# Kernel optimization log

Hardware: AMD Instinct MI355X
Metric: run time of the kernel (lower is better)

The kernel has to match this reference:

```python
import jax, jax.numpy as jnp
import numpy as np

N_NODES = 50000
N_EDGES = 800000
IN_CH = 128
HID = 32
HEADS = 4
OUT_CH = 16
NEG_SLOPE = 0.2  # PyG GATConv default LeakyReLU slope


def setup_inputs() -> dict:
    key = jax.random.key(0)
    ks = jax.random.split(key, 12)
    x = jax.random.normal(ks[0], (N_NODES, IN_CH), dtype=jnp.float32)
    edge_index = jax.random.randint(ks[1], (2, N_EDGES), 0, N_NODES, dtype=jnp.int32)
    edge_attr = jax.random.uniform(ks[2], (N_EDGES,), dtype=jnp.float32)
    s = 0.1
    W1 = jax.random.normal(ks[3], (IN_CH, HEADS * HID), dtype=jnp.float32) * s
    a_src1 = jax.random.normal(ks[4], (HEADS, HID), dtype=jnp.float32) * s
    a_dst1 = jax.random.normal(ks[5], (HEADS, HID), dtype=jnp.float32) * s
    b1 = jnp.zeros((HEADS * HID,), dtype=jnp.float32)
    W2 = jax.random.normal(ks[6], (HEADS * HID, OUT_CH), dtype=jnp.float32) * s
    a_src2 = jax.random.normal(ks[7], (1, OUT_CH), dtype=jnp.float32) * s
    a_dst2 = jax.random.normal(ks[8], (1, OUT_CH), dtype=jnp.float32) * s
    b2 = jnp.zeros((OUT_CH,), dtype=jnp.float32)
    return {"x": x, "edge_index": edge_index, "edge_attr": edge_attr,
            "W1": W1, "a_src1": a_src1, "a_dst1": a_dst1, "b1": b1,
            "W2": W2, "a_src2": a_src2, "a_dst2": a_dst2, "b2": b2}


def gat_conv(x, src, dst, num_nodes, W, a_src, a_dst, bias, concat):
    H, C = a_src.shape
    h = (x @ W).reshape(-1, H, C)              # [N,H,C]
    al_src = jnp.sum(h * a_src, axis=-1)       # [N,H]
    al_dst = jnp.sum(h * a_dst, axis=-1)       # [N,H]
    e = jax.nn.leaky_relu(al_src[src] + al_dst[dst], NEG_SLOPE)  # [E,H]
    # segment softmax over incoming edges of each destination node
    m = jax.ops.segment_max(e, dst, num_segments=num_nodes)
    ex = jnp.exp(e - m[dst])
    denom = jax.ops.segment_sum(ex, dst, num_segments=num_nodes)
    alpha = ex / (denom[dst] + 1e-16)          # [E,H]
    out = jax.ops.segment_sum(h[src] * alpha[..., None], dst, num_segments=num_nodes)  # [N,H,C]
    out = out.reshape(num_nodes, H * C) if concat else out.mean(axis=1)
    return out + bias


def reference(x, edge_index, edge_attr, W1, a_src1, a_dst1, b1, W2, a_src2, a_dst2, b2):
    # edge_attr is ignored by GATConv when edge_dim is None (PyG default)
    N = x.shape[0]
    loop = jnp.arange(N, dtype=edge_index.dtype)  # PyG add_self_loops=True
    src = jnp.concatenate([edge_index[0], loop])
    dst = jnp.concatenate([edge_index[1], loop])
    h = jax.nn.elu(gat_conv(x, src, dst, N, W1, a_src1, a_dst1, b1, True))
    out = gat_conv(h, src, dst, N, W2, a_src2, a_dst2, b2, False)
    return jax.nn.log_softmax(out, axis=1)
```

## Files before the change

kernel.cpp:

```cpp
#include <hip/hip_runtime.h>

#define N_NODESC 50000
#define E0C      800000
#define E_TOTC   850000
#define IN_CHC   128
#define HCC      128
#define HEADSC   4
#define OUT_CHC  16
#define NEG_SLOPE 0.2f
#define G1M      64
#define NG1      ((N_NODESC + G1M - 1)/G1M)
#define NBUCK    196
#define BNODES   256
#define SBLK     128
#define CHUNK    6656

typedef __attribute__((ext_vector_type(8))) short bf16x8;
typedef __attribute__((ext_vector_type(4))) float f32x4;

__device__ __forceinline__ float lrelu(float v){ return v > 0.f ? v : NEG_SLOPE * v; }

__device__ __forceinline__ unsigned int f2bf(float f){
  unsigned int b = __float_as_uint(f);
  return (b + 0x7fffu + ((b >> 16) & 1u)) >> 16;
}
__device__ __forceinline__ float bf2f(unsigned int lo16){
  return __uint_as_float(lo16 << 16);
}

__global__ void __launch_bounds__(256) k_gemm1A(const float* __restrict__ x, const float* __restrict__ W1,
        const float* __restrict__ a_s, const float* __restrict__ a_d,
        unsigned int* __restrict__ h1b, float* __restrict__ al_s, float* __restrict__ al_d,
        const int* __restrict__ ei, int* __restrict__ bh)
{
  __shared__ __align__(16) unsigned short Wt[IN_CHC*HCC];
  __shared__ __align__(16) unsigned short xt[G1M*IN_CHC];
  __shared__ int hh[NBUCK];
  int tid = threadIdx.x, lane = tid & 63, wave = tid >> 6;

  if (blockIdx.x >= NG1){
    int b = blockIdx.x - NG1;
    for (int i = tid; i < NBUCK; i += 256) hh[i] = 0;
    __syncthreads();
    int e0 = b*CHUNK, e1 = e0 + CHUNK; if (e1 > E_TOTC) e1 = E_TOTC;
    for (int e = e0 + tid; e < e1; e += 256){
      int d = (e < E0C) ? ei[E0C + e] : (e - E0C);
      atomicAdd(&hh[d >> 8], 1);
    }
    __syncthreads();
    for (int i = tid; i < NBUCK; i += 256) bh[b*NBUCK + i] = hh[i];
    return;
  }

  int row0 = blockIdx.x * G1M;
  for (int n0 = 0; n0 < 128; n0 += 64){
    int n = n0 + wave*16 + (lane & 15);
    for (int kc = 0; kc < 128; kc += 32){
      int k = kc + (lane >> 4)*8;
      unsigned int u[4];
      #pragma unroll
      for (int j = 0; j < 8; j += 2){
        float a = W1[(size_t)(k+j)*HCC + n];
        float b = W1[(size_t)(k+j+1)*HCC + n];
        u[j>>1] = f2bf(a) | (f2bf(b) << 16);
      }
      int idx = (n*128 + k) ^ ((n & 7) << 3);
      *(uint4*)&Wt[idx] = make_uint4(u[0],u[1],u[2],u[3]);
    }
  }
  {
    int r  = tid >> 2;
    int kc = (tid & 3) * 32;
    int rr = row0 + r; if (rr > N_NODESC-1) rr = N_NODESC-1;
    const float* xp = &x[(size_t)rr*IN_CHC + kc];
    #pragma unroll
    for (int j = 0; j < 32; j += 8){
      unsigned int u0 = f2bf(xp[j+0]) | (f2bf(xp[j+1]) << 16);
      unsigned int u1 = f2bf(xp[j+2]) | (f2bf(xp[j+3]) << 16);
      unsigned int u2 = f2bf(xp[j+4]) | (f2bf(xp[j+5]) << 16);
      unsigned int u3 = f2bf(xp[j+6]) | (f2bf(xp[j+7]) << 16);
      int idx = (r*128 + kc + j) ^ ((r & 7) << 3);
      *(uint4*)&xt[idx] = make_uint4(u0,u1,u2,u3);
    }
  }
  __syncthreads();

  int rw = wave * 16;
  f32x4 acc[8];
  #pragma unroll
  for (int t = 0; t < 8; t++) acc[t] = (f32x4){0.f,0.f,0.f,0.f};
  #pragma unroll
  for (int kk = 0; kk < 128; kk += 32){
    int m  = rw + (lane & 15);
    int ks = kk + (lane >> 4)*8;
    bf16x8 afrag = *(bf16x8*)&xt[(m*128 + ks) ^ ((m & 7) << 3)];
    #pragma unroll
    for (int t = 0; t < 8; t++){
      int n = t*16 + (lane & 15);
      bf16x8 bfrag = *(bf16x8*)&Wt[(n*128 + ks) ^ ((n & 7) << 3)];
      acc[t] = __builtin_amdgcn_mfma_f32_16x16x32_bf16(afrag, bfrag, acc[t], 0, 0, 0);
    }
  }

  float asv[8], adv[8];
  #pragma unroll
  for (int t = 0; t < 8; t++){
    asv[t] = a_s[t*16 + (lane & 15)];
    adv[t] = a_d[t*16 + (lane & 15)];
  }
  #pragma unroll
  for (int r = 0; r < 4; r++){
    int row = row0 + rw + (lane >> 4)*4 + r;
    bool ok = (row < N_NODESC);
    #pragma unroll
    for (int t = 0; t < 8; t++){
      float v = acc[t][r];
      float o = __shfl_xor(v, 1, 64);
      int c = t*16 + (lane & 15);
      if (ok && ((c & 1) == 0))
        h1b[(size_t)row*64 + (c >> 1)] = f2bf(v) | (f2bf(o) << 16);
    }
    #pragma unroll
    for (int h = 0; h < 4; h++){
      float ps = acc[2*h][r]*asv[2*h] + acc[2*h+1][r]*asv[2*h+1];
      float pd = acc[2*h][r]*adv[2*h] + acc[2*h+1][r]*adv[2*h+1];
      #pragma unroll
      for (int m = 1; m < 16; m <<= 1){ ps += __shfl_xor(ps, m, 64); pd += __shfl_xor(pd, m, 64); }
      if (ok && (lane & 15) == 0){
        al_s[row*HEADSC + h] = ps;
        al_d[row*HEADSC + h] = pd;
      }
    }
  }
}

__global__ void __launch_bounds__(256) k_binscan(int* __restrict__ bh, int* __restrict__ bstart){
  __shared__ int buf[256];
  int tid = threadIdx.x;
  int tot = 0;
  if (tid < NBUCK)
    for (int b = 0; b < SBLK; b++) tot += bh[b*NBUCK + tid];
  buf[tid] = (tid < NBUCK) ? tot : 0;
  __syncthreads();
  #pragma unroll
  for (int off = 1; off < 256; off <<= 1){
    int t = (tid >= off) ? buf[tid - off] : 0;
    __syncthreads();
    buf[tid] += t; __syncthreads();
  }
  int excl = buf[tid] - ((tid < NBUCK) ? tot : 0);
  if (tid < NBUCK) bstart[tid] = excl;
  if (tid == 0) bstart[NBUCK] = E_TOTC;
  __syncthreads();
  if (tid < NBUCK){
    int run = excl;
    for (int b = 0; b < SBLK; b++){
      int t = bh[b*NBUCK + tid];
      bh[b*NBUCK + tid] = run;
      run += t;
    }
  }
}

__global__ void __launch_bounds__(256) k_binB(const int* __restrict__ ei, const int* __restrict__ bh,
                                              unsigned int* __restrict__ binbuf){
  __shared__ int h[NBUCK];
  int tid = threadIdx.x, b = blockIdx.x;
  for (int i = tid; i < NBUCK; i += 256) h[i] = bh[b*NBUCK + i];
  __syncthreads();
  int e0 = b*CHUNK, e1 = e0 + CHUNK; if (e1 > E_TOTC) e1 = E_TOTC;
  for (int e = e0 + tid; e < e1; e += 256){
    int s, d;
    if (e < E0C){ d = ei[E0C + e]; s = ei[e]; }
    else { s = e - E0C; d = s; }
    int pos = atomicAdd(&h[d >> 8], 1);
    binbuf[pos] = ((unsigned int)d << 16) | (unsigned int)s;
  }
}

__global__ void __launch_bounds__(256) k_binC(const unsigned int* __restrict__ binbuf,
                                              const int* __restrict__ bstart,
                                              int* __restrict__ rp, unsigned short* __restrict__ srcs){
  __shared__ int lcnt[BNODES];
  __shared__ int buf[BNODES];
  __shared__ int pfx[BNODES];
  int tid = threadIdx.x, k = blockIdx.x;
  int lo = k * BNODES;
  int b0 = bstart[k], b1 = bstart[k+1];
  lcnt[tid] = 0;
  __syncthreads();
  for (int i = b0 + tid; i < b1; i += 256){
    int d = binbuf[i] >> 16;
    atomicAdd(&lcnt[d - lo], 1);
  }
  __syncthreads();
  int v = lcnt[tid];
  buf[tid] = v;
  __syncthreads();
  #pragma unroll
  for (int off = 1; off < 256; off <<= 1){
    int t = (tid >= off) ? buf[tid - off] : 0;
    __syncthreads();
    buf[tid] += t; __syncthreads();
  }
  int excl = buf[tid] - v;
  pfx[tid] = excl;
  int node = lo + tid;
  if (node < N_NODESC) rp[node] = b0 + excl;
  if (k == 0 && tid == 0) rp[N_NODESC] = E_TOTC;
  lcnt[tid] = 0;
  __syncthreads();
  for (int i = b0 + tid; i < b1; i += 256){
    unsigned int u = binbuf[i];
    int d = u >> 16;
    int r = atomicAdd(&lcnt[d - lo], 1);
    srcs[b0 + pfx[d - lo] + r] = (unsigned short)(u & 0xffffu);
  }
}

__global__ void __launch_bounds__(256) k_node1(const unsigned int* __restrict__ h1b,
        const float* __restrict__ al_s, const float* __restrict__ al_d,
        const int* __restrict__ rp, const unsigned short* __restrict__ srcs,
        const float* __restrict__ b1, unsigned int* __restrict__ houtb)
{
  int wave = threadIdx.x >> 6, lane = threadIdx.x & 63;
  int n = blockIdx.x*4 + wave;
  if (n >= N_NODESC) return;
  int beg = rp[n], end = rp[n+1];
  int h = lane >> 4;
  float adh = al_d[n*4 + h];
  float dsum = 0.f, acc0 = 0.f, acc1 = 0.f;
  #pragma unroll 4
  for (int p = beg; p < end; p++){
    int s = srcs[p];
    float a = __expf(lrelu(al_s[s*4 + h] + adh));
    unsigned int u = h1b[(size_t)s*64 + lane];
    dsum += a;
    acc0 = fmaf(a, bf2f(u & 0xffffu), acc0);
    acc1 = fmaf(a, bf2f(u >> 16), acc1);
  }
  float inv = 1.f / (dsum + 1e-16f);
  int c0 = lane*2;
  float o0 = acc0*inv + b1[c0], o1 = acc1*inv + b1[c0+1];
  o0 = o0 > 0.f ? o0 : __expf(o0) - 1.f;
  o1 = o1 > 0.f ? o1 : __expf(o1) - 1.f;
  houtb[(size_t)n*64 + lane] = f2bf(o0) | (f2bf(o1) << 16);
}

__global__ void __launch_bounds__(256) k_gemm2(const unsigned int* __restrict__ hinb, const float* __restrict__ W2,
        const float* __restrict__ a_s, const float* __restrict__ a_d,
        unsigned int* __restrict__ h2b, float* __restrict__ al_s, float* __restrict__ al_d)
{
  __shared__ __align__(16) float Wl[IN_CHC*OUT_CHC];
  __shared__ __align__(16) float xr[4][4][IN_CHC];
  int tid = threadIdx.x;
  for (int i = tid*4; i < IN_CHC*OUT_CHC; i += 256*4)
    *(float4*)&Wl[i] = *(const float4*)&W2[i];
  __syncthreads();
  int wave = tid >> 6, lane = tid & 63;
  int r = lane >> 4, c = lane & 15;
  int row0 = blockIdx.x*16 + wave*4;
  for (int rr = 0; rr < 4; rr++){
    unsigned int u = hinb[(size_t)(row0+rr)*64 + lane];
    xr[wave][rr][lane*2]   = bf2f(u & 0xffffu);
    xr[wave][rr][lane*2+1] = bf2f(u >> 16);
  }
  float acc = 0.f;
  #pragma unroll 8
  for (int k = 0; k < IN_CHC; k++)
    acc = fmaf(xr[wave][r][k], Wl[k*OUT_CHC + c], acc);
  int row = row0 + r;
  float other = __shfl_xor(acc, 1, 64);
  if ((c & 1) == 0)
    h2b[(size_t)row*8 + (c >> 1)] = f2bf(acc) | (f2bf(other) << 16);
  float ps = acc * a_s[c];
  float pd = acc * a_d[c];
  #pragma unroll
  for (int m = 1; m < 16; m <<= 1){ ps += __shfl_xor(ps, m, 64); pd += __shfl_xor(pd, m, 64); }
  if (c == 0){ al_s[row] = ps; al_d[row] = pd; }
}

__global__ void __launch_bounds__(256) k_node2(const unsigned int* __restrict__ h2b,
        const float* __restrict__ al_s, const float* __restrict__ al_d,
        const int* __restrict__ rp, const unsigned short* __restrict__ srcs,
        const float* __restrict__ b2, float* __restrict__ out)
{
  int wave = threadIdx.x >> 6, lane = threadIdx.x & 63;
  int n = blockIdx.x*4 + wave;
  if (n >= N_NODESC) return;
  int beg = rp[n], end = rp[n+1];
  float ad = al_d[n];
  int c = lane & 15, jg = lane >> 4;
  unsigned int hi = (c & 1);
  int widx = c >> 1;
  float dsum = 0.f, acc = 0.f;
  #pragma unroll 4
  for (int p = beg + jg; p < end; p += 4){
    int s = srcs[p];
    float a = __expf(lrelu(al_s[s] + ad));
    unsigned int u = h2b[(size_t)s*8 + widx];
    float hv = __uint_as_float(hi ? (u & 0xFFFF0000u) : (u << 16));
    dsum += a;
    acc = fmaf(a, hv, acc);
  }
  dsum += __shfl_xor(dsum, 16, 64);
  dsum += __shfl_xor(dsum, 32, 64);
  acc += __shfl_xor(acc, 16, 64);
  acc += __shfl_xor(acc, 32, 64);
  float inv = 1.f / (dsum + 1e-16f);
  float v = acc*inv + b2[c];
  float mm = v;
  #pragma unroll
  for (int o = 1; o < 16; o <<= 1) mm = fmaxf(mm, __shfl_xor(mm, o, 64));
  float se = __expf(v - mm);
  #pragma unroll
  for (int o = 1; o < 16; o <<= 1) se += __shfl_xor(se, o, 64);
  if (jg == 0) out[n*OUT_CHC + c] = v - mm - __logf(se);
}

extern "C" void kernel_launch(void* const* d_in, const int* in_sizes, int n_in,
                              void* d_out, int out_size, void* d_ws, size_t ws_size,
                              hipStream_t stream)
{
  const float* x   = (const float*)d_in[0];
  const int*   ei  = (const int*)d_in[1];
  const float* W1  = (const float*)d_in[3];
  const float* as1 = (const float*)d_in[4];
  const float* ad1 = (const float*)d_in[5];
  const float* b1  = (const float*)d_in[6];
  const float* W2  = (const float*)d_in[7];
  const float* as2 = (const float*)d_in[8];
  const float* ad2 = (const float*)d_in[9];
  const float* b2  = (const float*)d_in[10];
  float* out = (float*)d_out;

  char* ws = (char*)d_ws;
  size_t off = 0;
  auto alloc = [&](size_t bytes)->void*{
    void* p = ws + off;
    off = (off + bytes + 255) & ~(size_t)255;
    return p;
  };
  unsigned int* h1b = (unsigned int*)alloc((size_t)N_NODESC*64*4);
  unsigned int* houtb = (unsigned int*)alloc((size_t)N_NODESC*64*4);
  float* al_s1 = (float*)alloc((size_t)N_NODESC*HEADSC*4);
  float* al_d1 = (float*)alloc((size_t)N_NODESC*HEADSC*4);
  unsigned int* h2b = (unsigned int*)alloc((size_t)N_NODESC*8*4);
  float* al_s2 = (float*)alloc((size_t)N_NODESC*4);
  float* al_d2 = (float*)alloc((size_t)N_NODESC*4);
  int* rp      = (int*)alloc((size_t)(N_NODESC+1)*4);
  unsigned short* srcs = (unsigned short*)alloc((size_t)E_TOTC*2);
  int* bh      = (int*)alloc((size_t)SBLK*NBUCK*4);
  int* bstart  = (int*)alloc((size_t)(NBUCK+1)*4);
  unsigned int* binbuf = (unsigned int*)alloc((size_t)E_TOTC*4);

  k_gemm1A<<<NG1 + SBLK, 256, 0, stream>>>(x, W1, as1, ad1, h1b, al_s1, al_d1, ei, bh);
  k_binscan<<<1, 256, 0, stream>>>(bh, bstart);
  k_binB<<<SBLK, 256, 0, stream>>>(ei, bh, binbuf);
  k_binC<<<NBUCK, 256, 0, stream>>>(binbuf, bstart, rp, srcs);
  k_node1<<<N_NODESC/4, 256, 0, stream>>>(h1b, al_s1, al_d1, rp, srcs, b1, houtb);
  k_gemm2<<<N_NODESC/16, 256, 0, stream>>>(houtb, W2, as2, ad2, h2b, al_s2, al_d2);
  k_node2<<<N_NODESC/4, 256, 0, stream>>>(h2b, al_s2, al_d2, rp, srcs, b2, out);
}
```

Measured before the change: 140.0 us.

## Split layer-1 GEMM across the four CSR-build stages to overlap them

The layer-1 GEMM row blocks are divided into four slices, and each slice is co-launched with one of the CSR construction stages (bucket histogram, scan, bin scatter, per-node sort) in a single fused kernel. The serial, low-occupancy build kernels, especially the single-block scan, then share the GPU with GEMM work instead of running alone. The cost is that every launch carries the GEMM kernel's large shared memory footprint, which may lower occupancy for the CSR blocks. Stage-selection logic is also added, and the build stages reuse the GEMM tile buffer for their scratch space.

```diff
diff --git a/kernel.cpp b/kernel.cpp
--- a/kernel.cpp
+++ b/kernel.cpp
@@ -28,31 +28,104 @@
   return __uint_as_float(lo16 << 16);
 }
 
-__global__ void __launch_bounds__(256) k_gemm1A(const float* __restrict__ x, const float* __restrict__ W1,
+__global__ void __launch_bounds__(256) k_fused(const float* __restrict__ x, const float* __restrict__ W1,
         const float* __restrict__ a_s, const float* __restrict__ a_d,
         unsigned int* __restrict__ h1b, float* __restrict__ al_s, float* __restrict__ al_d,
-        const int* __restrict__ ei, int* __restrict__ bh)
+        const int* __restrict__ ei, int* __restrict__ bh, int* __restrict__ bstart,
+        unsigned int* __restrict__ binbuf, int* __restrict__ rp, unsigned short* __restrict__ srcs,
+        int gemmBase, int ngemm, int stage)
 {
   __shared__ __align__(16) unsigned short Wt[IN_CHC*HCC];
   __shared__ __align__(16) unsigned short xt[G1M*IN_CHC];
-  __shared__ int hh[NBUCK];
   int tid = threadIdx.x, lane = tid & 63, wave = tid >> 6;
 
-  if (blockIdx.x >= NG1){
-    int b = blockIdx.x - NG1;
-    for (int i = tid; i < NBUCK; i += 256) hh[i] = 0;
-    __syncthreads();
-    int e0 = b*CHUNK, e1 = e0 + CHUNK; if (e1 > E_TOTC) e1 = E_TOTC;
-    for (int e = e0 + tid; e < e1; e += 256){
-      int d = (e < E0C) ? ei[E0C + e] : (e - E0C);
-      atomicAdd(&hh[d >> 8], 1);
-    }
-    __syncthreads();
-    for (int i = tid; i < NBUCK; i += 256) bh[b*NBUCK + i] = hh[i];
+  if ((int)blockIdx.x >= ngemm){
+    int cb = blockIdx.x - ngemm;
+    int* sh = (int*)xt;
+    if (stage == 0){
+      for (int i = tid; i < NBUCK; i += 256) sh[i] = 0;
+      __syncthreads();
+      int e0 = cb*CHUNK, e1 = e0 + CHUNK; if (e1 > E_TOTC) e1 = E_TOTC;
+      for (int e = e0 + tid; e < e1; e += 256){
+        int d = (e < E0C) ? ei[E0C + e] : (e - E0C);
+        atomicAdd(&sh[d >> 8], 1);
+      }
+      __syncthreads();
+      for (int i = tid; i < NBUCK; i += 256) bh[cb*NBUCK + i] = sh[i];
+    } else if (stage == 1){
+      int tot = 0;
+      if (tid < NBUCK)
+        for (int b = 0; b < SBLK; b++) tot += bh[b*NBUCK + tid];
+      sh[tid] = (tid < NBUCK) ? tot : 0;
+      __syncthreads();
+      #pragma unroll
+      for (int off = 1; off < 256; off <<= 1){
+        int t = (tid >= off) ? sh[tid - off] : 0;
+        __syncthreads();
+        sh[tid] += t; __syncthreads();
+      }
+      int excl = sh[tid] - ((tid < NBUCK) ? tot : 0);
+      if (tid < NBUCK) bstart[tid] = excl;
+      if (tid == 0) bstart[NBUCK] = E_TOTC;
+      __syncthreads();
+      if (tid < NBUCK){
+        int run = excl;
+        for (int b = 0; b < SBLK; b++){
+          int t = bh[b*NBUCK + tid];
+          bh[b*NBUCK + tid] = run;
+          run += t;
+        }
+      }
+    } else if (stage == 2){
+      for (int i = tid; i < NBUCK; i += 256) sh[i] = bh[cb*NBUCK + i];
+      __syncthreads();
+      int e0 = cb*CHUNK, e1 = e0 + CHUNK; if (e1 > E_TOTC) e1 = E_TOTC;
+      for (int e = e0 + tid; e < e1; e += 256){
+        int s, d;
+        if (e < E0C){ d = ei[E0C + e]; s = ei[e]; }
+        else { s = e - E0C; d = s; }
+        int pos = atomicAdd(&sh[d >> 8], 1);
+        binbuf[pos] = ((unsigned int)d << 16) | (unsigned int)s;
+      }
+    } else {
+      int* lcnt = sh; int* buf = sh + 256; int* pfx = sh + 512;
+      int k = cb;
+      int lo = k * BNODES;
+      int b0 = bstart[k], b1 = bstart[k+1];
+      lcnt[tid] = 0;
+      __syncthreads();
+      for (int i = b0 + tid; i < b1; i += 256){
+        int d = binbuf[i] >> 16;
+        atomicAdd(&lcnt[d - lo], 1);
+      }
+      __syncthreads();
+      int v = lcnt[tid];
+      buf[tid] = v;
+      __syncthreads();
+      #pragma unroll
+      for (int off = 1; off < 256; off <<= 1){
+        int t = (tid >= off) ? buf[tid - off] : 0;
+        __syncthreads();
+        buf[tid] += t; __syncthreads();
+      }
+      int excl = buf[tid] - v;
+      pfx[tid] = excl;
+      int node = lo + tid;
+      if (node < N_NODESC) rp[node] = b0 + excl;
+      if (k == 0 && tid == 0) rp[N_NODESC] = E_TOTC;
+      lcnt[tid] = 0;
+      __syncthreads();
+      for (int i = b0 + tid; i < b1; i += 256){
+        unsigned int u = binbuf[i];
+        int d = u >> 16;
+        int r = atomicAdd(&lcnt[d - lo], 1);
+        srcs[b0 + pfx[d - lo] + r] = (unsigned short)(u & 0xffffu);
+      }
+    }
     return;
   }
 
-  int row0 = blockIdx.x * G1M;
+  int row0 = (gemmBase + blockIdx.x) * G1M;
   for (int n0 = 0; n0 < 128; n0 += 64){
     int n = n0 + wave*16 + (lane & 15);
     for (int kc = 0; kc < 128; kc += 32){
@@ -131,90 +204,6 @@
         al_d[row*HEADSC + h] = pd;
       }
     }
-  }
-}
-
-__global__ void __launch_bounds__(256) k_binscan(int* __restrict__ bh, int* __restrict__ bstart){
-  __shared__ int buf[256];
-  int tid = threadIdx.x;
-  int tot = 0;
-  if (tid < NBUCK)
-    for (int b = 0; b < SBLK; b++) tot += bh[b*NBUCK + tid];
-  buf[tid] = (tid < NBUCK) ? tot : 0;
-  __syncthreads();
-  #pragma unroll
-  for (int off = 1; off < 256; off <<= 1){
-    int t = (tid >= off) ? buf[tid - off] : 0;
-    __syncthreads();
-    buf[tid] += t; __syncthreads();
-  }
-  int excl = buf[tid] - ((tid < NBUCK) ? tot : 0);
-  if (tid < NBUCK) bstart[tid] = excl;
-  if (tid == 0) bstart[NBUCK] = E_TOTC;
-  __syncthreads();
-  if (tid < NBUCK){
-    int run = excl;
-    for (int b = 0; b < SBLK; b++){
-      int t = bh[b*NBUCK + tid];
-      bh[b*NBUCK + tid] = run;
-      run += t;
-    }
-  }
-}
-
-__global__ void __launch_bounds__(256) k_binB(const int* __restrict__ ei, const int* __restrict__ bh,
-                                              unsigned int* __restrict__ binbuf){
-  __shared__ int h[NBUCK];
-  int tid = threadIdx.x, b = blockIdx.x;
-  for (int i = tid; i < NBUCK; i += 256) h[i] = bh[b*NBUCK + i];
-  __syncthreads();
-  int e0 = b*CHUNK, e1 = e0 + CHUNK; if (e1 > E_TOTC) e1 = E_TOTC;
-  for (int e = e0 + tid; e < e1; e += 256){
-    int s, d;
-    if (e < E0C){ d = ei[E0C + e]; s = ei[e]; }
-    else { s = e - E0C; d = s; }
-    int pos = atomicAdd(&h[d >> 8], 1);
-    binbuf[pos] = ((unsigned int)d << 16) | (unsigned int)s;
-  }
-}
-
-__global__ void __launch_bounds__(256) k_binC(const unsigned int* __restrict__ binbuf,
-                                              const int* __restrict__ bstart,
-                                              int* __restrict__ rp, unsigned short* __restrict__ srcs){
-  __shared__ int lcnt[BNODES];
-  __shared__ int buf[BNODES];
-  __shared__ int pfx[BNODES];
-  int tid = threadIdx.x, k = blockIdx.x;
-  int lo = k * BNODES;
-  int b0 = bstart[k], b1 = bstart[k+1];
-  lcnt[tid] = 0;
-  __syncthreads();
-  for (int i = b0 + tid; i < b1; i += 256){
-    int d = binbuf[i] >> 16;
-    atomicAdd(&lcnt[d - lo], 1);
-  }
-  __syncthreads();
-  int v = lcnt[tid];
-  buf[tid] = v;
-  __syncthreads();
-  #pragma unroll
-  for (int off = 1; off < 256; off <<= 1){
-    int t = (tid >= off) ? buf[tid - off] : 0;
-    __syncthreads();
-    buf[tid] += t; __syncthreads();
-  }
-  int excl = buf[tid] - v;
-  pfx[tid] = excl;
-  int node = lo + tid;
-  if (node < N_NODESC) rp[node] = b0 + excl;
-  if (k == 0 && tid == 0) rp[N_NODESC] = E_TOTC;
-  lcnt[tid] = 0;
-  __syncthreads();
-  for (int i = b0 + tid; i < b1; i += 256){
-    unsigned int u = binbuf[i];
-    int d = u >> 16;
-    int r = atomicAdd(&lcnt[d - lo], 1);
-    srcs[b0 + pfx[d - lo] + r] = (unsigned short)(u & 0xffffu);
   }
 }
 
@@ -354,10 +343,14 @@
   int* bstart  = (int*)alloc((size_t)(NBUCK+1)*4);
   unsigned int* binbuf = (unsigned int*)alloc((size_t)E_TOTC*4);
 
-  k_gemm1A<<<NG1 + SBLK, 256, 0, stream>>>(x, W1, as1, ad1, h1b, al_s1, al_d1, ei, bh);
-  k_binscan<<<1, 256, 0, stream>>>(bh, bstart);
-  k_binB<<<SBLK, 256, 0, stream>>>(ei, bh, binbuf);
-  k_binC<<<NBUCK, 256, 0, stream>>>(binbuf, bstart, rp, srcs);
+  k_fused<<<196 + SBLK, 256, 0, stream>>>(x, W1, as1, ad1, h1b, al_s1, al_d1,
+        ei, bh, bstart, binbuf, rp, srcs, 0, 196, 0);
+  k_fused<<<196 + 1, 256, 0, stream>>>(x, W1, as1, ad1, h1b, al_s1, al_d1,
+        ei, bh, bstart, binbuf, rp, srcs, 196, 196, 1);
+  k_fused<<<196 + SBLK, 256, 0, stream>>>(x, W1, as1, ad1, h1b, al_s1, al_d1,
+        ei, bh, bstart, binbuf, rp, srcs, 392, 196, 2);
+  k_fused<<<194 + NBUCK, 256, 0, stream>>>(x, W1, as1, ad1, h1b, al_s1, al_d1,
+        ei, bh, bstart, binbuf, rp, srcs, 588, 194, 3);
   k_node1<<<N_NODESC/4, 256, 0, stream>>>(h1b, al_s1, al_d1, rp, srcs, b1, houtb);
   k_gemm2<<<N_NODESC/16, 256, 0, stream>>>(houtb, W2, as2, ad2, h2b, al_s2, al_d2);
   k_node2<<<N_NODESC/4, 256, 0, stream>>>(h2b, al_s2, al_d2, rp, srcs, b2, out);
```

Result: no change. 137.5 us, median of 2 (-1.8%).
